# Kernel tuning notes

Measured on AMD Instinct MI355X. Metric: run time of the kernel, lower is better.

## Reference

```python
import jax, jax.numpy as jnp
import numpy as np

N_NODES = 100000
N_EDGES = 800000
HIDDEN = 128


def setup_inputs() -> dict:
    key = jax.random.key(0)
    k1, k2, k3, k4, k5, k6 = jax.random.split(key, 6)
    z = jax.random.normal(k1, (N_NODES, HIDDEN), dtype=jnp.float32)
    edge_index = jax.random.randint(k2, (2, N_EDGES), 0, N_NODES, dtype=jnp.int64)
    # nn.Linear params (torch default init scale ~ 1/sqrt(fan_in))
    s1 = 1.0 / np.sqrt(2 * HIDDEN)
    s2 = 1.0 / np.sqrt(HIDDEN)
    W1 = jax.random.uniform(k3, (2 * HIDDEN, HIDDEN), jnp.float32, -s1, s1)
    b1 = jax.random.uniform(k4, (HIDDEN,), jnp.float32, -s1, s1)
    W2 = jax.random.uniform(k5, (HIDDEN, 1), jnp.float32, -s2, s2)
    b2 = jax.random.uniform(k6, (1,), jnp.float32, -s2, s2)
    return {"z": z, "edge_index": edge_index, "W1": W1, "b1": b1, "W2": W2, "b2": b2}


def reference(z, edge_index, W1, b1, W2, b2):
    src, dst = edge_index[0], edge_index[1]
    # Gather endpoint features: [E, H] each. Avoid materializing the [E, 2H]
    # concat by splitting W1 into src/dst halves (same math as cat + matmul).
    W1_src, W1_dst = W1[:HIDDEN], W1[HIDDEN:]
    h = z[src] @ W1_src + z[dst] @ W1_dst + b1  # [E, H]
    h = jax.nn.relu(h)
    score = h @ W2 + b2  # [E, 1]
    return score
```

## Files before the change

### kernel.cpp

```cpp
#include <hip/hip_runtime.h>
#include <hip/hip_bf16.h>

#define N_NODES 100000
#define N_EDGES 800000
#define HIDDEN 128
#define N_TILES 1563
#define PC_GRID 512

typedef short frag_ab __attribute__((ext_vector_type(8)));
typedef float frag_cd __attribute__((ext_vector_type(4)));

__device__ inline unsigned short f2b(float f) {
    union { float f; unsigned u; } x; x.f = f;
    return (unsigned short)((x.u + 0x7fffu + ((x.u >> 16) & 1u)) >> 16);
}

__device__ inline unsigned pk2(float x, float y) {
    union { __hip_bfloat162 h; unsigned u; } c;
    c.h = __float22bfloat162_rn(make_float2(x, y));
    return c.u;
}

__global__ __launch_bounds__(256) void transpose_w1(
    const float* __restrict__ W1, unsigned short* __restrict__ Bt)
{
    const int t  = threadIdx.x;
    const int nc = blockIdx.x * 4 + (t >> 6);
    const int k2 = (t & 63) * 2;
    const int col  = nc & 127;
    const int roff = (nc >= 128) ? 128 : 0;
    float f0 = W1[(size_t)(roff + k2)     * HIDDEN + col];
    float f1 = W1[(size_t)(roff + k2 + 1) * HIDDEN + col];
    *(unsigned*)(Bt + (size_t)nc * HIDDEN + k2) = (unsigned)f2b(f0) | ((unsigned)f2b(f1) << 16);
}

#define AS_STRIDE 136

__global__ __launch_bounds__(256) void precompute_uv_mfma(
    const float* __restrict__ z, const unsigned short* __restrict__ Bt,
    const float* __restrict__ b1, unsigned char* __restrict__ UVq,
    float* __restrict__ scales)
{
    __shared__ float smemf[64 * 256];
    unsigned short* smem = (unsigned short*)smemf;
    const int t = threadIdx.x;
    const int lane = t & 63;
    const int w = t >> 6;
    const int wn = w * 64;
    const int g  = lane >> 4;
    const int lc = lane & 15;

    frag_ab b[4][4];
    float bias[4];
    #pragma unroll
    for (int nt = 0; nt < 4; ++nt) {
        int nc = wn + nt * 16 + lc;
        bias[nt] = (nc < HIDDEN) ? b1[nc] : 0.f;
        const unsigned short* brow = Bt + (size_t)nc * HIDDEN;
        #pragma unroll
        for (int q = 0; q < 4; ++q)
            b[nt][q] = *(const frag_ab*)(brow + q * 32 + g * 8);
    }

    int tile = blockIdx.x;
    uint2 pf[8];
    #pragma unroll
    for (int i = 0; i < 8; ++i) {
        int f4 = i * 256 + t;
        int m = tile * 64 + (f4 >> 5);
        if (m >= N_NODES) m = N_NODES - 1;
        float4 v = ((const float4*)z)[(size_t)m * 32 + (f4 & 31)];
        pf[i].x = pk2(v.x, v.y);
        pf[i].y = pk2(v.z, v.w);
    }

    while (true) {
        #pragma unroll
        for (int i = 0; i < 8; ++i) {
            int f4 = i * 256 + t;
            *(uint2*)&smem[(f4 >> 5) * AS_STRIDE + (f4 & 31) * 4] = pf[i];
        }
        __syncthreads();

        const int next = tile + PC_GRID;
        const bool have_next = (next < N_TILES);
        if (have_next) {
            #pragma unroll
            for (int i = 0; i < 8; ++i) {
                int f4 = i * 256 + t;
                int m = next * 64 + (f4 >> 5);
                if (m >= N_NODES) m = N_NODES - 1;
                float4 v = ((const float4*)z)[(size_t)m * 32 + (f4 & 31)];
                pf[i].x = pk2(v.x, v.y);
                pf[i].y = pk2(v.z, v.w);
            }
        }

        frag_cd acc[4][4];
        #pragma unroll
        for (int mt = 0; mt < 4; ++mt)
            #pragma unroll
            for (int nt = 0; nt < 4; ++nt)
                acc[mt][nt] = (frag_cd){0.f, 0.f, 0.f, 0.f};
        #pragma unroll
        for (int q = 0; q < 4; ++q) {
            frag_ab a[4];
            #pragma unroll
            for (int mt = 0; mt < 4; ++mt)
                a[mt] = *(const frag_ab*)&smem[(mt * 16 + lc) * AS_STRIDE + q * 32 + g * 8];
            #pragma unroll
            for (int mt = 0; mt < 4; ++mt)
                #pragma unroll
                for (int nt = 0; nt < 4; ++nt)
                    acc[mt][nt] = __builtin_amdgcn_mfma_f32_16x16x32_bf16(
                        a[mt], b[nt][q], acc[mt][nt], 0, 0, 0);
        }
        __syncthreads();

        #pragma unroll
        for (int nt = 0; nt < 4; ++nt) {
            int nc = wn + nt * 16 + lc;
            #pragma unroll
            for (int mt = 0; mt < 4; ++mt)
                #pragma unroll
                for (int r = 0; r < 4; ++r) {
                    int row = mt * 16 + g * 4 + r;
                    smemf[row * 256 + (nc ^ (g << 4))] = acc[mt][nt][r] + bias[nt];
                }
        }
        __syncthreads();

        const int m0 = tile * 64;
        #pragma unroll
        for (int it = 0; it < 16; ++it) {
            const int row  = it * 4 + w;
            const int node = m0 + row;
            const int c    = (it & 3) << 4;
            float4 x = *(const float4*)&smemf[row * 256 + ((lane * 4) ^ c)];
            float mx = fmaxf(fmaxf(fabsf(x.x), fabsf(x.y)),
                             fmaxf(fabsf(x.z), fabsf(x.w)));
            #pragma unroll
            for (int k = 1; k < 32; k <<= 1)
                mx = fmaxf(mx, __shfl_xor(mx, k, 32));
            mx = fmaxf(mx, 1e-12f);
            const float ainv = 127.0f / mx;
            unsigned q0 = (unsigned)__builtin_fmaf(x.x, ainv, 128.5f);
            unsigned q1 = (unsigned)__builtin_fmaf(x.y, ainv, 128.5f);
            unsigned q2 = (unsigned)__builtin_fmaf(x.z, ainv, 128.5f);
            unsigned q3 = (unsigned)__builtin_fmaf(x.w, ainv, 128.5f);
            unsigned pack = q0 | (q1 << 8) | (q2 << 16) | (q3 << 24);
            if (node < N_NODES) {
                *(unsigned*)&UVq[(size_t)node * 256 + lane * 4] = pack;
                if ((lane & 31) == 0)
                    scales[node * 2 + (lane >> 5)] = mx * (1.0f / 127.0f);
            }
        }

        if (!have_next) break;
        __syncthreads();
        tile = next;
    }
}

__device__ inline float dq4(unsigned uq, unsigned vq, float aU, float aV,
                            float k, float4 w, float acc) {
    #pragma unroll
    for (int b = 0; b < 4; ++b) {
        float uf = (float)((uq >> (8 * b)) & 0xffu);
        float vf = (float)((vq >> (8 * b)) & 0xffu);
        float h  = __builtin_fmaf(aU, uf, __builtin_fmaf(aV, vf, k));
        h = fmaxf(h, 0.f);
        float wv = (b == 0) ? w.x : (b == 1) ? w.y : (b == 2) ? w.z : w.w;
        acc = __builtin_fmaf(h, wv, acc);
    }
    return acc;
}

__global__ __launch_bounds__(256) void edge_score(
    const int* __restrict__ ei, const unsigned char* __restrict__ UVq,
    const float* __restrict__ scales, const float* __restrict__ W2,
    const float* __restrict__ B2, float* __restrict__ out)
{
    const int t = threadIdx.x;
    const int g = t & 7;
    const int slot = t >> 3;
    const int e0 = blockIdx.x * 64 + slot;
    const int e1 = e0 + 32;

    const float4* W24 = (const float4*)W2;
    const float4 w0 = W24[g * 4 + 0];
    const float4 w1 = W24[g * 4 + 1];
    const float4 w2 = W24[g * 4 + 2];
    const float4 w3 = W24[g * 4 + 3];

    const int s0 = ei[e0];
    const int d0 = ei[N_EDGES + e0];
    const int s1 = ei[e1];
    const int d1 = ei[N_EDGES + e1];

    const uint4 u0 = *(const uint4*)(UVq + (size_t)s0 * 256 + g * 16);
    const uint4 v0 = *(const uint4*)(UVq + (size_t)d0 * 256 + 128 + g * 16);
    const uint4 u1 = *(const uint4*)(UVq + (size_t)s1 * 256 + g * 16);
    const uint4 v1 = *(const uint4*)(UVq + (size_t)d1 * 256 + 128 + g * 16);
    const float aU0 = scales[s0 * 2];
    const float aV0 = scales[d0 * 2 + 1];
    const float aU1 = scales[s1 * 2];
    const float aV1 = scales[d1 * 2 + 1];

    const float k0 = -128.f * (aU0 + aV0);
    const float k1 = -128.f * (aU1 + aV1);

    float A = 0.f, B = 0.f;
    A = dq4(u0.x, v0.x, aU0, aV0, k0, w0, A);
    A = dq4(u0.y, v0.y, aU0, aV0, k0, w1, A);
    A = dq4(u0.z, v0.z, aU0, aV0, k0, w2, A);
    A = dq4(u0.w, v0.w, aU0, aV0, k0, w3, A);

    B = dq4(u1.x, v1.x, aU1, aV1, k1, w0, B);
    B = dq4(u1.y, v1.y, aU1, aV1, k1, w1, B);
    B = dq4(u1.z, v1.z, aU1, aV1, k1, w2, B);
    B = dq4(u1.w, v1.w, aU1, aV1, k1, w3, B);

    float sa = A;
    float sb = B;
    sa += __shfl_xor(sa, 1, 8);
    sa += __shfl_xor(sa, 2, 8);
    sa += __shfl_xor(sa, 4, 8);
    sb += __shfl_xor(sb, 1, 8);
    sb += __shfl_xor(sb, 2, 8);
    sb += __shfl_xor(sb, 4, 8);

    if (g == 0) {
        float bb = B2[0];
        out[e0] = sa + bb;
        out[e1] = sb + bb;
    }
}

extern "C" void kernel_launch(void* const* d_in, const int* in_sizes, int n_in,
                              void* d_out, int out_size, void* d_ws, size_t ws_size,
                              hipStream_t stream) {
    const float* z  = (const float*)d_in[0];
    const int*   ei = (const int*)d_in[1];
    const float* W1 = (const float*)d_in[2];
    const float* b1 = (const float*)d_in[3];
    const float* W2 = (const float*)d_in[4];
    const float* b2 = (const float*)d_in[5];
    float* out = (float*)d_out;

    unsigned char* UVq = (unsigned char*)d_ws;
    float* scales = (float*)(UVq + (size_t)N_NODES * 256);
    unsigned short* Bt = (unsigned short*)(scales + 2 * N_NODES);

    transpose_w1<<<64, 256, 0, stream>>>(W1, Bt);
    precompute_uv_mfma<<<PC_GRID, 256, 0, stream>>>(z, Bt, b1, UVq, scales);
    edge_score<<<N_EDGES / 64, 256, 0, stream>>>(ei, UVq, scales, W2, b2, out);
}
```

Before: 147.4 us.

## Quantize precompute outputs from registers via transposed MFMA and partial row maxima

```diff
diff --git a/kernel.cpp b/kernel.cpp
--- a/kernel.cpp
+++ b/kernel.cpp
@@ -36,37 +36,40 @@
 
 #define AS_STRIDE 136
 
-__global__ __launch_bounds__(256) void precompute_uv_mfma(
+__global__ __launch_bounds__(512, 4) void precompute_uv_mfma(
     const float* __restrict__ z, const unsigned short* __restrict__ Bt,
     const float* __restrict__ b1, unsigned char* __restrict__ UVq,
     float* __restrict__ scales)
 {
-    __shared__ float smemf[64 * 256];
-    unsigned short* smem = (unsigned short*)smemf;
+    __shared__ unsigned short smem[64 * AS_STRIDE];
+    __shared__ float ppart[8 * 64];
     const int t = threadIdx.x;
     const int lane = t & 63;
     const int w = t >> 6;
-    const int wn = w * 64;
+    const int wm = w * 32;
     const int g  = lane >> 4;
     const int lc = lane & 15;
-
-    frag_ab b[4][4];
-    float bias[4];
+    const int grp = w >> 2;
+
+    frag_ab b[2][4];
+    float bias[2][4];
     #pragma unroll
-    for (int nt = 0; nt < 4; ++nt) {
-        int nc = wn + nt * 16 + lc;
-        bias[nt] = (nc < HIDDEN) ? b1[nc] : 0.f;
+    for (int mt = 0; mt < 2; ++mt) {
+        const int nc = wm + mt * 16 + lc;
         const unsigned short* brow = Bt + (size_t)nc * HIDDEN;
         #pragma unroll
         for (int q = 0; q < 4; ++q)
-            b[nt][q] = *(const frag_ab*)(brow + q * 32 + g * 8);
+            b[mt][q] = *(const frag_ab*)(brow + q * 32 + g * 8);
+        #pragma unroll
+        for (int r = 0; r < 4; ++r)
+            bias[mt][r] = (w < 4) ? b1[wm + mt * 16 + g * 4 + r] : 0.f;
     }
 
     int tile = blockIdx.x;
-    uint2 pf[8];
+    uint2 pf[4];
     #pragma unroll
-    for (int i = 0; i < 8; ++i) {
-        int f4 = i * 256 + t;
+    for (int i = 0; i < 4; ++i) {
+        int f4 = i * 512 + t;
         int m = tile * 64 + (f4 >> 5);
         if (m >= N_NODES) m = N_NODES - 1;
         float4 v = ((const float4*)z)[(size_t)m * 32 + (f4 & 31)];
@@ -76,8 +79,8 @@
 
     while (true) {
         #pragma unroll
-        for (int i = 0; i < 8; ++i) {
-            int f4 = i * 256 + t;
+        for (int i = 0; i < 4; ++i) {
+            int f4 = i * 512 + t;
             *(uint2*)&smem[(f4 >> 5) * AS_STRIDE + (f4 & 31) * 4] = pf[i];
         }
         __syncthreads();
@@ -86,8 +89,8 @@
         const bool have_next = (next < N_TILES);
         if (have_next) {
             #pragma unroll
-            for (int i = 0; i < 8; ++i) {
-                int f4 = i * 256 + t;
+            for (int i = 0; i < 4; ++i) {
+                int f4 = i * 512 + t;
                 int m = next * 64 + (f4 >> 5);
                 if (m >= N_NODES) m = N_NODES - 1;
                 float4 v = ((const float4*)z)[(size_t)m * 32 + (f4 & 31)];
@@ -96,9 +99,9 @@
             }
         }
 
-        frag_cd acc[4][4];
-        #pragma unroll
-        for (int mt = 0; mt < 4; ++mt)
+        frag_cd acc[2][4];
+        #pragma unroll
+        for (int mt = 0; mt < 2; ++mt)
             #pragma unroll
             for (int nt = 0; nt < 4; ++nt)
                 acc[mt][nt] = (frag_cd){0.f, 0.f, 0.f, 0.f};
@@ -106,58 +109,63 @@
         for (int q = 0; q < 4; ++q) {
             frag_ab a[4];
             #pragma unroll
-            for (int mt = 0; mt < 4; ++mt)
-                a[mt] = *(const frag_ab*)&smem[(mt * 16 + lc) * AS_STRIDE + q * 32 + g * 8];
-            #pragma unroll
-            for (int mt = 0; mt < 4; ++mt)
+            for (int nt = 0; nt < 4; ++nt)
+                a[nt] = *(const frag_ab*)&smem[(nt * 16 + lc) * AS_STRIDE + q * 32 + g * 8];
+            #pragma unroll
+            for (int mt = 0; mt < 2; ++mt)
                 #pragma unroll
                 for (int nt = 0; nt < 4; ++nt)
                     acc[mt][nt] = __builtin_amdgcn_mfma_f32_16x16x32_bf16(
-                        a[mt], b[nt][q], acc[mt][nt], 0, 0, 0);
+                        b[mt][q], a[nt], acc[mt][nt], 0, 0, 0);
+        }
+
+        const int m0 = tile * 64;
+        float red[4];
+        #pragma unroll
+        for (int nt = 0; nt < 4; ++nt) {
+            float mx = 0.f;
+            #pragma unroll
+            for (int mt = 0; mt < 2; ++mt)
+                #pragma unroll
+                for (int r = 0; r < 4; ++r)
+                    mx = fmaxf(mx, fabsf(acc[mt][nt][r] + bias[mt][r]));
+            mx = fmaxf(mx, __shfl_xor(mx, 16));
+            mx = fmaxf(mx, __shfl_xor(mx, 32));
+            red[nt] = mx;
+        }
+        if (g == 0) {
+            #pragma unroll
+            for (int nt = 0; nt < 4; ++nt)
+                ppart[w * 64 + nt * 16 + lc] = red[nt];
         }
         __syncthreads();
 
         #pragma unroll
         for (int nt = 0; nt < 4; ++nt) {
-            int nc = wn + nt * 16 + lc;
-            #pragma unroll
-            for (int mt = 0; mt < 4; ++mt)
-                #pragma unroll
-                for (int r = 0; r < 4; ++r) {
-                    int row = mt * 16 + g * 4 + r;
-                    smemf[row * 256 + (nc ^ (g << 4))] = acc[mt][nt][r] + bias[nt];
-                }
-        }
-        __syncthreads();
-
-        const int m0 = tile * 64;
-        #pragma unroll
-        for (int it = 0; it < 16; ++it) {
-            const int row  = it * 4 + w;
-            const int node = m0 + row;
-            const int c    = (it & 3) << 4;
-            float4 x = *(const float4*)&smemf[row * 256 + ((lane * 4) ^ c)];
-            float mx = fmaxf(fmaxf(fabsf(x.x), fabsf(x.y)),
-                             fmaxf(fabsf(x.z), fabsf(x.w)));
-            #pragma unroll
-            for (int k = 1; k < 32; k <<= 1)
-                mx = fmaxf(mx, __shfl_xor(mx, k, 32));
+            const int idx  = nt * 16 + lc;
+            const int node = m0 + idx;
+            float mx = fmaxf(fmaxf(ppart[(grp * 4 + 0) * 64 + idx],
+                                   ppart[(grp * 4 + 1) * 64 + idx]),
+                             fmaxf(ppart[(grp * 4 + 2) * 64 + idx],
+                                   ppart[(grp * 4 + 3) * 64 + idx]));
             mx = fmaxf(mx, 1e-12f);
             const float ainv = 127.0f / mx;
-            unsigned q0 = (unsigned)__builtin_fmaf(x.x, ainv, 128.5f);
-            unsigned q1 = (unsigned)__builtin_fmaf(x.y, ainv, 128.5f);
-            unsigned q2 = (unsigned)__builtin_fmaf(x.z, ainv, 128.5f);
-            unsigned q3 = (unsigned)__builtin_fmaf(x.w, ainv, 128.5f);
-            unsigned pack = q0 | (q1 << 8) | (q2 << 16) | (q3 << 24);
             if (node < N_NODES) {
-                *(unsigned*)&UVq[(size_t)node * 256 + lane * 4] = pack;
-                if ((lane & 31) == 0)
-                    scales[node * 2 + (lane >> 5)] = mx * (1.0f / 127.0f);
+                #pragma unroll
+                for (int mt = 0; mt < 2; ++mt) {
+                    unsigned q0 = (unsigned)__builtin_fmaf(acc[mt][nt][0] + bias[mt][0], ainv, 128.5f);
+                    unsigned q1 = (unsigned)__builtin_fmaf(acc[mt][nt][1] + bias[mt][1], ainv, 128.5f);
+                    unsigned q2 = (unsigned)__builtin_fmaf(acc[mt][nt][2] + bias[mt][2], ainv, 128.5f);
+                    unsigned q3 = (unsigned)__builtin_fmaf(acc[mt][nt][3] + bias[mt][3], ainv, 128.5f);
+                    unsigned pack = q0 | (q1 << 8) | (q2 << 16) | (q3 << 24);
+                    *(unsigned*)&UVq[(size_t)node * 256 + wm + mt * 16 + g * 4] = pack;
+                }
+                if (g == 0 && (w == 0 || w == 4))
+                    scales[node * 2 + grp] = mx * (1.0f / 127.0f);
             }
         }
 
         if (!have_next) break;
-        __syncthreads();
         tile = next;
     }
 }
@@ -253,6 +261,6 @@
     unsigned short* Bt = (unsigned short*)(scales + 2 * N_NODES);
 
     transpose_w1<<<64, 256, 0, stream>>>(W1, Bt);
-    precompute_uv_mfma<<<PC_GRID, 256, 0, stream>>>(z, Bt, b1, UVq, scales);
+    precompute_uv_mfma<<<PC_GRID, 512, 0, stream>>>(z, Bt, b1, UVq, scales);
     edge_score<<<N_EDGES / 64, 256, 0, stream>>>(ei, UVq, scales, W2, b2, out);
 }
```

Result: faster. 142.7 us (-3.2%).

## Compute node projections transposed per wave, dropping LDS staging and persistent loop

Applied to the files above, without the earlier changes.

```diff
diff --git a/kernel.cpp b/kernel.cpp
--- a/kernel.cpp
+++ b/kernel.cpp
@@ -4,8 +4,6 @@
 #define N_NODES 100000
 #define N_EDGES 800000
 #define HIDDEN 128
-#define N_TILES 1563
-#define PC_GRID 512
 
 typedef short frag_ab __attribute__((ext_vector_type(8)));
 typedef float frag_cd __attribute__((ext_vector_type(4)));
@@ -34,131 +32,88 @@
     *(unsigned*)(Bt + (size_t)nc * HIDDEN + k2) = (unsigned)f2b(f0) | ((unsigned)f2b(f1) << 16);
 }
 
-#define AS_STRIDE 136
-
 __global__ __launch_bounds__(256) void precompute_uv_mfma(
     const float* __restrict__ z, const unsigned short* __restrict__ Bt,
     const float* __restrict__ b1, unsigned char* __restrict__ UVq,
     float* __restrict__ scales)
 {
-    __shared__ float smemf[64 * 256];
-    unsigned short* smem = (unsigned short*)smemf;
     const int t = threadIdx.x;
     const int lane = t & 63;
     const int w = t >> 6;
-    const int wn = w * 64;
     const int g  = lane >> 4;
     const int lc = lane & 15;
 
-    frag_ab b[4][4];
-    float bias[4];
-    #pragma unroll
-    for (int nt = 0; nt < 4; ++nt) {
-        int nc = wn + nt * 16 + lc;
-        bias[nt] = (nc < HIDDEN) ? b1[nc] : 0.f;
-        const unsigned short* brow = Bt + (size_t)nc * HIDDEN;
+    const int gid = blockIdx.x * 4 + w;
+    if (gid >= N_NODES / 16) return;
+    const int node = gid * 16 + lc;
+
+    const float4* zrow = (const float4*)z + (size_t)node * 32;
+    frag_ab zf[4];
+    #pragma unroll
+    for (int q = 0; q < 4; ++q) {
+        float4 v0 = zrow[q * 8 + g * 2];
+        float4 v1 = zrow[q * 8 + g * 2 + 1];
+        union { unsigned u[4]; frag_ab f; } pk;
+        pk.u[0] = pk2(v0.x, v0.y);
+        pk.u[1] = pk2(v0.z, v0.w);
+        pk.u[2] = pk2(v1.x, v1.y);
+        pk.u[3] = pk2(v1.z, v1.w);
+        zf[q] = pk.f;
+    }
+
+    frag_cd acc[16];
+    #pragma unroll
+    for (int mt = 0; mt < 16; ++mt)
+        acc[mt] = (frag_cd){0.f, 0.f, 0.f, 0.f};
+    #pragma unroll
+    for (int q = 0; q < 4; ++q) {
         #pragma unroll
-        for (int q = 0; q < 4; ++q)
-            b[nt][q] = *(const frag_ab*)(brow + q * 32 + g * 8);
-    }
-
-    int tile = blockIdx.x;
-    uint2 pf[8];
-    #pragma unroll
-    for (int i = 0; i < 8; ++i) {
-        int f4 = i * 256 + t;
-        int m = tile * 64 + (f4 >> 5);
-        if (m >= N_NODES) m = N_NODES - 1;
-        float4 v = ((const float4*)z)[(size_t)m * 32 + (f4 & 31)];
-        pf[i].x = pk2(v.x, v.y);
-        pf[i].y = pk2(v.z, v.w);
-    }
-
-    while (true) {
+        for (int mt = 0; mt < 16; ++mt) {
+            frag_ab wf = *(const frag_ab*)(Bt + (size_t)(mt * 16 + lc) * HIDDEN
+                                              + q * 32 + g * 8);
+            acc[mt] = __builtin_amdgcn_mfma_f32_16x16x32_bf16(wf, zf[q], acc[mt], 0, 0, 0);
+        }
+    }
+
+    const float4* b1f4 = (const float4*)b1;
+    float mxU = 0.f, mxV = 0.f;
+    #pragma unroll
+    for (int mt = 0; mt < 8; ++mt) {
+        float4 bb = b1f4[mt * 4 + g];
+        acc[mt][0] += bb.x; acc[mt][1] += bb.y;
+        acc[mt][2] += bb.z; acc[mt][3] += bb.w;
         #pragma unroll
-        for (int i = 0; i < 8; ++i) {
-            int f4 = i * 256 + t;
-            *(uint2*)&smem[(f4 >> 5) * AS_STRIDE + (f4 & 31) * 4] = pf[i];
-        }
-        __syncthreads();
-
-        const int next = tile + PC_GRID;
-        const bool have_next = (next < N_TILES);
-        if (have_next) {
-            #pragma unroll
-            for (int i = 0; i < 8; ++i) {
-                int f4 = i * 256 + t;
-                int m = next * 64 + (f4 >> 5);
-                if (m >= N_NODES) m = N_NODES - 1;
-                float4 v = ((const float4*)z)[(size_t)m * 32 + (f4 & 31)];
-                pf[i].x = pk2(v.x, v.y);
-                pf[i].y = pk2(v.z, v.w);
-            }
-        }
-
-        frag_cd acc[4][4];
+        for (int r = 0; r < 4; ++r)
+            mxU = fmaxf(mxU, fabsf(acc[mt][r]));
+    }
+    #pragma unroll
+    for (int mt = 8; mt < 16; ++mt)
         #pragma unroll
-        for (int mt = 0; mt < 4; ++mt)
-            #pragma unroll
-            for (int nt = 0; nt < 4; ++nt)
-                acc[mt][nt] = (frag_cd){0.f, 0.f, 0.f, 0.f};
-        #pragma unroll
-        for (int q = 0; q < 4; ++q) {
-            frag_ab a[4];
-            #pragma unroll
-            for (int mt = 0; mt < 4; ++mt)
-                a[mt] = *(const frag_ab*)&smem[(mt * 16 + lc) * AS_STRIDE + q * 32 + g * 8];
-            #pragma unroll
-            for (int mt = 0; mt < 4; ++mt)
-                #pragma unroll
-                for (int nt = 0; nt < 4; ++nt)
-                    acc[mt][nt] = __builtin_amdgcn_mfma_f32_16x16x32_bf16(
-                        a[mt], b[nt][q], acc[mt][nt], 0, 0, 0);
-        }
-        __syncthreads();
-
-        #pragma unroll
-        for (int nt = 0; nt < 4; ++nt) {
-            int nc = wn + nt * 16 + lc;
-            #pragma unroll
-            for (int mt = 0; mt < 4; ++mt)
-                #pragma unroll
-                for (int r = 0; r < 4; ++r) {
-                    int row = mt * 16 + g * 4 + r;
-                    smemf[row * 256 + (nc ^ (g << 4))] = acc[mt][nt][r] + bias[nt];
-                }
-        }
-        __syncthreads();
-
-        const int m0 = tile * 64;
-        #pragma unroll
-        for (int it = 0; it < 16; ++it) {
-            const int row  = it * 4 + w;
-            const int node = m0 + row;
-            const int c    = (it & 3) << 4;
-            float4 x = *(const float4*)&smemf[row * 256 + ((lane * 4) ^ c)];
-            float mx = fmaxf(fmaxf(fabsf(x.x), fabsf(x.y)),
-                             fmaxf(fabsf(x.z), fabsf(x.w)));
-            #pragma unroll
-            for (int k = 1; k < 32; k <<= 1)
-                mx = fmaxf(mx, __shfl_xor(mx, k, 32));
-            mx = fmaxf(mx, 1e-12f);
-            const float ainv = 127.0f / mx;
-            unsigned q0 = (unsigned)__builtin_fmaf(x.x, ainv, 128.5f);
-            unsigned q1 = (unsigned)__builtin_fmaf(x.y, ainv, 128.5f);
-            unsigned q2 = (unsigned)__builtin_fmaf(x.z, ainv, 128.5f);
-            unsigned q3 = (unsigned)__builtin_fmaf(x.w, ainv, 128.5f);
-            unsigned pack = q0 | (q1 << 8) | (q2 << 16) | (q3 << 24);
-            if (node < N_NODES) {
-                *(unsigned*)&UVq[(size_t)node * 256 + lane * 4] = pack;
-                if ((lane & 31) == 0)
-                    scales[node * 2 + (lane >> 5)] = mx * (1.0f / 127.0f);
-            }
-        }
-
-        if (!have_next) break;
-        __syncthreads();
-        tile = next;
+        for (int r = 0; r < 4; ++r)
+            mxV = fmaxf(mxV, fabsf(acc[mt][r]));
+
+    mxU = fmaxf(mxU, __shfl_xor(mxU, 16));
+    mxU = fmaxf(mxU, __shfl_xor(mxU, 32));
+    mxV = fmaxf(mxV, __shfl_xor(mxV, 16));
+    mxV = fmaxf(mxV, __shfl_xor(mxV, 32));
+    mxU = fmaxf(mxU, 1e-12f);
+    mxV = fmaxf(mxV, 1e-12f);
+    const float ainvU = 127.0f / mxU;
+    const float ainvV = 127.0f / mxV;
+
+    unsigned char* urow = UVq + (size_t)node * 256;
+    #pragma unroll
+    for (int mt = 0; mt < 16; ++mt) {
+        const float ainv = (mt < 8) ? ainvU : ainvV;
+        unsigned q0 = (unsigned)__builtin_fmaf(acc[mt][0], ainv, 128.5f);
+        unsigned q1 = (unsigned)__builtin_fmaf(acc[mt][1], ainv, 128.5f);
+        unsigned q2 = (unsigned)__builtin_fmaf(acc[mt][2], ainv, 128.5f);
+        unsigned q3 = (unsigned)__builtin_fmaf(acc[mt][3], ainv, 128.5f);
+        *(unsigned*)&urow[mt * 16 + g * 4] = q0 | (q1 << 8) | (q2 << 16) | (q3 << 24);
+    }
+    if (g == 0) {
+        scales[node * 2 + 0] = mxU * (1.0f / 127.0f);
+        scales[node * 2 + 1] = mxV * (1.0f / 127.0f);
     }
 }
 
@@ -253,6 +208,6 @@
     unsigned short* Bt = (unsigned short*)(scales + 2 * N_NODES);
 
     transpose_w1<<<64, 256, 0, stream>>>(W1, Bt);
-    precompute_uv_mfma<<<PC_GRID, 256, 0, stream>>>(z, Bt, b1, UVq, scales);
+    precompute_uv_mfma<<<(N_NODES / 16 + 3) / 4, 256, 0, stream>>>(z, Bt, b1, UVq, scales);
     edge_score<<<N_EDGES / 64, 256, 0, stream>>>(ei, UVq, scales, W2, b2, out);
 }
```

Result: slower. 182.0 us (+23.5%).
